# Kernel tuning notes

Hardware: AMD Instinct MI355X
Metric: run time of the kernel (lower is better)

Reference implementation:

```python
import jax, jax.numpy as jnp
import numpy as np

B, S, E, H = 2, 2048, 1024, 16  # batch, max_seq_length, embedding_dim, num_heads
D = E // H  # head dim = 64


def setup_inputs() -> dict:
    key = jax.random.key(0)
    ks = jax.random.split(key, 7)
    scale = 0.02
    return {
        "inputs": jax.random.normal(ks[0], (B, S, E), jnp.float32),
        "embbeding_V": jax.random.normal(ks[1], (B, S, E), jnp.float32),
        "embbeding_K": jax.random.normal(ks[2], (B, S, E), jnp.float32),
        "Wq": jax.random.normal(ks[3], (E, E), jnp.float32) * scale,
        "Wk": jax.random.normal(ks[4], (E, E), jnp.float32) * scale,
        "Wv": jax.random.normal(ks[5], (E, E), jnp.float32) * scale,
        "Wo": jax.random.normal(ks[6], (E, E), jnp.float32) * scale,
    }


def reference(inputs, embbeding_V, embbeding_K, Wq, Wk, Wv, Wo):
    b = inputs.shape[0]
    # repeat last token of `inputs` to max_seq_length: [b, S, E]
    x = jnp.broadcast_to(inputs[:, -1, :][:, None, :], (b, S, E))
    # torch Linear(bias=False): y = x @ W.T ; split heads -> [b, H, S, D]
    q = (x @ Wq.T).reshape(b, S, H, D).transpose(0, 2, 1, 3)
    k = (embbeding_K @ Wk.T).reshape(b, S, H, D).transpose(0, 2, 1, 3)
    v = (embbeding_V @ Wv.T).reshape(b, S, H, D).transpose(0, 2, 1, 3)
    # UNSCALED attention (faithful to source: no 1/sqrt(d))
    s = jnp.einsum("bhqd,bhkd->bhqk", q, k)
    p = jax.nn.softmax(s, axis=-1)
    o = jnp.einsum("bhqk,bhkd->bhqd", p, v)
    # transpose(1,2) then reshape to [b, S, E]
    o = o.transpose(0, 2, 1, 3).reshape(b, S, E)
    return o @ Wo.T
```

## Files before the change

### kernel.cpp

```cpp
#include <hip/hip_runtime.h>
#include <hip/hip_bf16.h>

constexpr int B = 2, S = 2048, E = 1024, H = 16, D = 64;
constexpr int E4 = E / 4;

__global__ __launch_bounds__(256) void k_qwkq(const float4* __restrict__ x4,
                                              const float4* __restrict__ Wq4,
                                              const float* __restrict__ Wk,
                                              float* __restrict__ wkq,
                                              float* __restrict__ rowsum) {
  int b = blockIdx.x, h = blockIdx.y, eo = blockIdx.z;
  int t = threadIdx.x;
  __shared__ float qred[64][4];
  __shared__ float qh[64];
  const float4* xr = x4 + ((size_t)b * S + (S - 1)) * E4;
  {
    int n = t >> 2, part = t & 3;
    const float4* wr = Wq4 + (size_t)(h * 64 + n) * E4 + part * 64;
    const float4* xp = xr + part * 64;
    float acc = 0.f;
#pragma unroll 8
    for (int j = 0; j < 64; ++j) {
      float4 a = xp[j], w = wr[j];
      acc += a.x * w.x + a.y * w.y + a.z * w.z + a.w * w.w;
    }
    qred[n][part] = acc;
  }
  __syncthreads();
  if (t < 64) qh[t] = qred[t][0] + qred[t][1] + qred[t][2] + qred[t][3];
  if (t == 0 && eo == 0) rowsum[b * H + h] = 0.f;
  __syncthreads();
  int e = eo * 512 + t;
  const float* wp = Wk + (size_t)(h * 64) * E + e;
  float a0 = 0.f, a1 = 0.f;
#pragma unroll 8
  for (int d = 0; d < 64; ++d) {
    float q = qh[d];
    a0 += q * wp[(size_t)d * E];
    a1 += q * wp[(size_t)d * E + 256];
  }
  int bh = b * H + h;
  wkq[(size_t)bh * E + e] = a0;
  wkq[(size_t)bh * E + e + 256] = a1;
}

__global__ __launch_bounds__(256) void k_scores_exp(const float4* __restrict__ embK,
                                                    const float4* __restrict__ wkq4,
                                                    float* __restrict__ p,
                                                    float* __restrict__ rowsum) {
  __shared__ float4 wl[H * E4];
  __shared__ float hsum[16];
  int blk = blockIdx.x;
  int b = blk >> 7, k0 = (blk & 127) * 16;
  int tid = threadIdx.x;
#pragma unroll
  for (int j = 0; j < 16; ++j)
    wl[j * 256 + tid] = wkq4[(size_t)b * (H * E4) + j * 256 + tid];
  if (tid < 16) hsum[tid] = 0.f;
  __syncthreads();
  int k = tid >> 4, es = tid & 15;
  const float4* er = embK + ((size_t)b * S + k0 + k) * E4;
  float4 v[16];
#pragma unroll
  for (int j = 0; j < 16; ++j) v[j] = er[es + 16 * j];
#pragma unroll 1
  for (int h = 0; h < H; ++h) {
    float acc = 0.f;
#pragma unroll
    for (int j = 0; j < 16; ++j) {
      float4 w = wl[h * 256 + es + 16 * j];
      acc += v[j].x * w.x + v[j].y * w.y + v[j].z * w.z + v[j].w * w.w;
    }
#pragma unroll
    for (int o = 8; o > 0; o >>= 1) acc += __shfl_xor(acc, o, 64);
    if (es == 0) {
      float pe = __expf(acc);
      p[((size_t)(b * H + h)) * S + k0 + k] = pe;
      atomicAdd(&hsum[h], pe);
    }
  }
  __syncthreads();
  if (tid < 16) atomicAdd(&rowsum[b * H + tid], hsum[tid]);
}

__global__ __launch_bounds__(256) void k_ctx_part(const float4* __restrict__ embV,
                                                  const float* __restrict__ p,
                                                  const float* __restrict__ rowsum,
                                                  float4* __restrict__ part) {
  int b = blockIdx.x, eo = blockIdx.y, kz = blockIdx.z;
  int tid = threadIdx.x;
  int e4l = tid & 63, w = tid >> 6;
  int k0 = kz * 128;
  __shared__ float pl[16 * 128];
  __shared__ float sinv[16];
  if (tid < 16) sinv[tid] = 1.f / rowsum[b * H + tid];
  __syncthreads();
  for (int i = tid; i < 16 * 128; i += 256) {
    int h = i >> 7, kk = i & 127;
    pl[i] = p[((size_t)(b * H + h)) * S + k0 + kk] * sinv[h];
  }
  __syncthreads();
  int e4 = eo * 64 + e4l;
  float4 acc[H];
#pragma unroll
  for (int h = 0; h < H; ++h) acc[h] = make_float4(0.f, 0.f, 0.f, 0.f);
  int kb = w * 32;
  for (int i = 0; i < 32; ++i) {
    int kk = kb + i;
    float4 v = embV[((size_t)b * S + k0 + kk) * E4 + e4];
#pragma unroll
    for (int h = 0; h < H; ++h) {
      float pv = pl[h * 128 + kk];
      acc[h].x += pv * v.x; acc[h].y += pv * v.y;
      acc[h].z += pv * v.z; acc[h].w += pv * v.w;
    }
  }
  int pz = kz * 4 + w;
#pragma unroll
  for (int h = 0; h < H; ++h)
    part[((size_t)(pz * B + b) * H + h) * E4 + e4] = acc[h];
}

__global__ __launch_bounds__(256) void k_ovec(const float4* __restrict__ part,
                                              const float4* __restrict__ Wv4,
                                              float* __restrict__ o_vec) {
  int b = blockIdx.x, h = blockIdx.y;
  int t = threadIdx.x;
  __shared__ float4 crow[E4];
  float4 acc = make_float4(0.f, 0.f, 0.f, 0.f);
  const float4* pp = part + ((size_t)b * H + h) * E4 + t;
  const size_t pstride = (size_t)B * H * E4;
#pragma unroll 8
  for (int pz = 0; pz < 64; ++pz) {
    float4 c = pp[pz * pstride];
    acc.x += c.x; acc.y += c.y; acc.z += c.z; acc.w += c.w;
  }
  crow[t] = acc;
  __syncthreads();
  int n_l = t >> 2, p4 = t & 3;
  const float4* wr = Wv4 + (size_t)(h * 64 + n_l) * E4 + p4 * 64;
  float a = 0.f;
#pragma unroll 8
  for (int j = 0; j < 64; ++j) {
    float4 c = crow[p4 * 64 + j];
    float4 w = wr[j];
    a += c.x * w.x + c.y * w.y + c.z * w.z + c.w * w.w;
  }
  a += __shfl_xor(a, 1, 64);
  a += __shfl_xor(a, 2, 64);
  if (p4 == 0) o_vec[(size_t)b * E + h * 64 + n_l] = a;
}

__global__ void k_outvec(const float* __restrict__ o_vec, const float4* __restrict__ Wo4,
                         float* __restrict__ out_vec) {
  int gw = (blockIdx.x * blockDim.x + threadIdx.x) >> 6;
  int lane = threadIdx.x & 63;
  int b = gw >> 10, nn = gw & 1023;
  const float4* xr = (const float4*)(o_vec + (size_t)b * E);
  const float4* wr = Wo4 + (size_t)nn * E4;
  float acc = 0.f;
#pragma unroll
  for (int j = 0; j < 4; ++j) {
    float4 a = xr[lane + 64 * j];
    float4 w = wr[lane + 64 * j];
    acc += a.x * w.x + a.y * w.y + a.z * w.z + a.w * w.w;
  }
#pragma unroll
  for (int o = 32; o > 0; o >>= 1) acc += __shfl_xor(acc, o, 64);
  if (lane == 0) out_vec[gw] = acc;
}

__global__ void k_bcast(const float4* __restrict__ ov4, float4* __restrict__ out4) {
  int base = blockIdx.x * 1024 + threadIdx.x;
#pragma unroll
  for (int r = 0; r < 4; ++r) {
    int g = base + r * 256;
    out4[g] = ov4[(g >> 19) * E4 + (g & 255)];
  }
}

extern "C" void kernel_launch(void* const* d_in, const int* in_sizes, int n_in,
                              void* d_out, int out_size, void* d_ws, size_t ws_size,
                              hipStream_t stream) {
  const float* inputs = (const float*)d_in[0];
  const float* embV   = (const float*)d_in[1];
  const float* embK   = (const float*)d_in[2];
  const float* Wq     = (const float*)d_in[3];
  const float* Wk     = (const float*)d_in[4];
  const float* Wv     = (const float*)d_in[5];
  const float* Wo     = (const float*)d_in[6];

  float* ws      = (float*)d_ws;
  float* wkq     = ws;
  float* p       = wkq + B * H * E;
  float* rowsum  = p + B * H * S;
  float* o_vec   = rowsum + 64;
  float* out_vec = o_vec + B * E;
  float* part    = out_vec + B * E;

  k_qwkq<<<dim3(B, H, 2), 256, 0, stream>>>((const float4*)inputs, (const float4*)Wq,
                                            Wk, wkq, rowsum);
  k_scores_exp<<<256, 256, 0, stream>>>((const float4*)embK, (const float4*)wkq,
                                        p, rowsum);
  k_ctx_part<<<dim3(B, 4, 16), 256, 0, stream>>>((const float4*)embV, p, rowsum,
                                                 (float4*)part);
  k_ovec<<<dim3(B, H), 256, 0, stream>>>((const float4*)part, (const float4*)Wv, o_vec);
  k_outvec<<<512, 256, 0, stream>>>(o_vec, (const float4*)Wo, out_vec);
  k_bcast<<<1024, 256, 0, stream>>>((const float4*)out_vec, (float4*)d_out);
}
```

Baseline: 162.4 us.

## Split q/Wk·q kernel into wider-grid kernels and halve scores block size

The fused q-projection plus Wk^T·q kernel ran on only 64 blocks, and each block recomputed q. It is replaced by two kernels: a 256-block q_vec GEMV and a 256-block wkq kernel with 128 threads each. The scores kernel now uses 128 threads, each handling two key rows, so the Wk·q row loaded from LDS is reused across two keys, at the cost of more registers per thread. This adds one extra kernel launch and a global round-trip for q_vec.

```diff
diff --git a/kernel.cpp b/kernel.cpp
--- a/kernel.cpp
+++ b/kernel.cpp
@@ -4,47 +4,46 @@
 constexpr int B = 2, S = 2048, E = 1024, H = 16, D = 64;
 constexpr int E4 = E / 4;
 
-__global__ __launch_bounds__(256) void k_qwkq(const float4* __restrict__ x4,
-                                              const float4* __restrict__ Wq4,
-                                              const float* __restrict__ Wk,
-                                              float* __restrict__ wkq,
-                                              float* __restrict__ rowsum) {
-  int b = blockIdx.x, h = blockIdx.y, eo = blockIdx.z;
-  int t = threadIdx.x;
-  __shared__ float qred[64][4];
-  __shared__ float qh[64];
-  const float4* xr = x4 + ((size_t)b * S + (S - 1)) * E4;
-  {
-    int n = t >> 2, part = t & 3;
-    const float4* wr = Wq4 + (size_t)(h * 64 + n) * E4 + part * 64;
-    const float4* xp = xr + part * 64;
-    float acc = 0.f;
+__global__ void k_qvec(const float4* __restrict__ x, const float4* __restrict__ Wq,
+                       float* __restrict__ q_vec) {
+  int blk = blockIdx.x;
+  int b = blk >> 7, n0 = (blk & 127) * 8;
+  int tid = threadIdx.x;
+  int nl = tid >> 5, es = tid & 31;
+  const float4* xr = x + ((size_t)b * S + (S - 1)) * E4;
+  const float4* wr = Wq + (size_t)(n0 + nl) * E4;
+  float acc = 0.f;
+#pragma unroll
+  for (int j = 0; j < 8; ++j) {
+    float4 a = xr[es + 32 * j];
+    float4 w = wr[es + 32 * j];
+    acc += a.x * w.x + a.y * w.y + a.z * w.z + a.w * w.w;
+  }
+#pragma unroll
+  for (int o = 16; o > 0; o >>= 1) acc += __shfl_xor(acc, o, 64);
+  if (es == 0) q_vec[b * E + n0 + nl] = acc;
+}
+
+__global__ void k_wkq(const float* __restrict__ q_vec, const float* __restrict__ Wk,
+                      float* __restrict__ wkq, float* __restrict__ rowsum) {
+  int blk = blockIdx.x;
+  int eo = blk & 7;
+  int bh = blk >> 3;
+  int h = bh & 15;
+  int tid = threadIdx.x;
+  __shared__ float qh[D];
+  if (tid < D) qh[tid] = q_vec[(bh >> 4) * E + h * D + tid];
+  if (eo == 0 && tid == 0) rowsum[bh] = 0.f;
+  __syncthreads();
+  int e = eo * 128 + tid;
+  const float* wp = Wk + (size_t)h * D * E + e;
+  float acc = 0.f;
 #pragma unroll 8
-    for (int j = 0; j < 64; ++j) {
-      float4 a = xp[j], w = wr[j];
-      acc += a.x * w.x + a.y * w.y + a.z * w.z + a.w * w.w;
-    }
-    qred[n][part] = acc;
-  }
-  __syncthreads();
-  if (t < 64) qh[t] = qred[t][0] + qred[t][1] + qred[t][2] + qred[t][3];
-  if (t == 0 && eo == 0) rowsum[b * H + h] = 0.f;
-  __syncthreads();
-  int e = eo * 512 + t;
-  const float* wp = Wk + (size_t)(h * 64) * E + e;
-  float a0 = 0.f, a1 = 0.f;
-#pragma unroll 8
-  for (int d = 0; d < 64; ++d) {
-    float q = qh[d];
-    a0 += q * wp[(size_t)d * E];
-    a1 += q * wp[(size_t)d * E + 256];
-  }
-  int bh = b * H + h;
-  wkq[(size_t)bh * E + e] = a0;
-  wkq[(size_t)bh * E + e + 256] = a1;
-}
-
-__global__ __launch_bounds__(256) void k_scores_exp(const float4* __restrict__ embK,
+  for (int d = 0; d < D; ++d) acc += qh[d] * wp[(size_t)d * E];
+  wkq[(size_t)bh * E + e] = acc;
+}
+
+__global__ __launch_bounds__(128) void k_scores_exp(const float4* __restrict__ embK,
                                                     const float4* __restrict__ wkq4,
                                                     float* __restrict__ p,
                                                     float* __restrict__ rowsum) {
@@ -54,29 +53,37 @@
   int b = blk >> 7, k0 = (blk & 127) * 16;
   int tid = threadIdx.x;
 #pragma unroll
-  for (int j = 0; j < 16; ++j)
-    wl[j * 256 + tid] = wkq4[(size_t)b * (H * E4) + j * 256 + tid];
+  for (int j = 0; j < 32; ++j)
+    wl[j * 128 + tid] = wkq4[(size_t)b * (H * E4) + j * 128 + tid];
   if (tid < 16) hsum[tid] = 0.f;
   __syncthreads();
-  int k = tid >> 4, es = tid & 15;
-  const float4* er = embK + ((size_t)b * S + k0 + k) * E4;
-  float4 v[16];
-#pragma unroll
-  for (int j = 0; j < 16; ++j) v[j] = er[es + 16 * j];
+  int kp = tid >> 4, es = tid & 15;
+  int ka = k0 + kp, kb = k0 + 8 + kp;
+  const float4* ea = embK + ((size_t)b * S + ka) * E4;
+  const float4* eb = embK + ((size_t)b * S + kb) * E4;
+  float4 va[16], vb[16];
+#pragma unroll
+  for (int j = 0; j < 16; ++j) { va[j] = ea[es + 16 * j]; vb[j] = eb[es + 16 * j]; }
 #pragma unroll 1
   for (int h = 0; h < H; ++h) {
-    float acc = 0.f;
+    float aa = 0.f, ab = 0.f;
 #pragma unroll
     for (int j = 0; j < 16; ++j) {
       float4 w = wl[h * 256 + es + 16 * j];
-      acc += v[j].x * w.x + v[j].y * w.y + v[j].z * w.z + v[j].w * w.w;
-    }
-#pragma unroll
-    for (int o = 8; o > 0; o >>= 1) acc += __shfl_xor(acc, o, 64);
+      aa += va[j].x * w.x + va[j].y * w.y + va[j].z * w.z + va[j].w * w.w;
+      ab += vb[j].x * w.x + vb[j].y * w.y + vb[j].z * w.z + vb[j].w * w.w;
+    }
+#pragma unroll
+    for (int o = 8; o > 0; o >>= 1) {
+      aa += __shfl_xor(aa, o, 64);
+      ab += __shfl_xor(ab, o, 64);
+    }
     if (es == 0) {
-      float pe = __expf(acc);
-      p[((size_t)(b * H + h)) * S + k0 + k] = pe;
-      atomicAdd(&hsum[h], pe);
+      float pa = __expf(aa), pb = __expf(ab);
+      float* pr = p + ((size_t)(b * H + h)) * S;
+      pr[ka] = pa;
+      pr[kb] = pb;
+      atomicAdd(&hsum[h], pa + pb);
     }
   }
   __syncthreads();
@@ -191,16 +198,17 @@
   const float* Wo     = (const float*)d_in[6];
 
   float* ws      = (float*)d_ws;
-  float* wkq     = ws;
+  float* q_vec   = ws;
+  float* wkq     = q_vec + B * E;
   float* p       = wkq + B * H * E;
   float* rowsum  = p + B * H * S;
   float* o_vec   = rowsum + 64;
   float* out_vec = o_vec + B * E;
   float* part    = out_vec + B * E;
 
-  k_qwkq<<<dim3(B, H, 2), 256, 0, stream>>>((const float4*)inputs, (const float4*)Wq,
-                                            Wk, wkq, rowsum);
-  k_scores_exp<<<256, 256, 0, stream>>>((const float4*)embK, (const float4*)wkq,
+  k_qvec<<<256, 256, 0, stream>>>((const float4*)inputs, (const float4*)Wq, q_vec);
+  k_wkq<<<256, 128, 0, stream>>>(q_vec, Wk, wkq, rowsum);
+  k_scores_exp<<<256, 128, 0, stream>>>((const float4*)embK, (const float4*)wkq,
                                         p, rowsum);
   k_ctx_part<<<dim3(B, 4, 16), 256, 0, stream>>>((const float4*)embV, p, rowsum,
                                                  (float4*)part);
```

Result: faster. 156.7 us (-3.5%).
